# Performance work log

Hardware: AMD Instinct MI355X
Metric: run time of the kernel (lower is better)

## Reference

```python
import jax, jax.numpy as jnp
import numpy as np

H, W, C = 32, 32, 3
KH, KW, KC = 4, 4, 3
SHIFT = (2, 2)
K = 48
M = 200
NH, NW, NC = H // KH, W // KW, C // KC  # 8, 8, 1
NKERNEL = NH * NW * NC                  # 64
NDIM_SUB = KH * KW * KC                 # 48
NDIM = H * W * C                        # 3072
NTR = NKERNEL * K                       # 3072
N = 8192


def setup_inputs() -> dict:
    key = jax.random.key(0)
    ks = jax.random.split(key, 7)
    data = jax.random.normal(ks[0], (N, NDIM), jnp.float32)
    A_raw = jax.random.normal(ks[1], (NKERNEL, NDIM_SUB, K), jnp.float32)
    # RQspline params: knots span roughly [-5, 5]
    x0 = -5.0 + 0.1 * jax.random.normal(ks[2], (NTR, 1), jnp.float32)
    logdx = jnp.log(10.0 / (M - 1)) + 0.1 * jax.random.normal(ks[3], (NTR, M - 1), jnp.float32)
    y0 = -5.0 + 0.1 * jax.random.normal(ks[4], (NTR, 1), jnp.float32)
    logdy = jnp.log(10.0 / (M - 1)) + 0.1 * jax.random.normal(ks[5], (NTR, M - 1), jnp.float32)
    logderiv = 0.1 * jax.random.normal(ks[6], (NTR, M), jnp.float32)
    return {"data": data, "A_raw": A_raw, "x0": x0, "logdx": logdx,
            "y0": y0, "logdy": logdy, "logderiv": logderiv}


def _patch_dims():
    # Shift() is a circular roll of the flat-index image toward the origin
    dim = jnp.arange(NDIM).reshape(H, W, C)
    dim = jnp.roll(dim, shift=(-SHIFT[0], -SHIFT[1]), axis=(0, 1))
    # (NH,KH,NW,KW,C) -> (NH,NW,KH,KW,C) -> (NKERNEL, NDIM_SUB)
    return dim.reshape(NH, KH, NW, KW, C).transpose(0, 2, 1, 3, 4).reshape(NKERNEL, NDIM_SUB)


def orthogonalize(A_raw):
    # per-patch QR with sign fix, as in __init__
    Q, R = jnp.linalg.qr(A_raw)
    sign = jnp.sign(jnp.diagonal(R, axis1=-2, axis2=-1))
    return Q * sign[:, None, :]


def construct_A(A_blocks):
    rows = _patch_dims()                                               # (NKERNEL, NDIM_SUB)
    cols = K * jnp.arange(NKERNEL)[:, None] + jnp.arange(K)[None, :]   # (NKERNEL, K)
    Afull = jnp.zeros((NDIM, NTR), A_blocks.dtype)
    return Afull.at[rows[:, :, None], cols[:, None, :]].set(A_blocks)


def rqspline_forward(x, x0, logdx, y0, logdy, logderiv):
    # monotone rational-quadratic spline (Gregory-Delbourgo), per-dim knots
    xx = jnp.concatenate([x0, x0 + jnp.cumsum(jnp.exp(logdx), axis=1)], axis=1)  # (NTR, M)
    yy = jnp.concatenate([y0, y0 + jnp.cumsum(jnp.exp(logdy), axis=1)], axis=1)
    delta = jnp.exp(logderiv)
    xT = x.T                                              # (NTR, N)
    idx = jax.vmap(jnp.searchsorted)(xx, xT)              # (NTR, N)
    k = jnp.clip(idx - 1, 0, M - 2)
    xK = jnp.take_along_axis(xx, k, axis=1)
    xK1 = jnp.take_along_axis(xx, k + 1, axis=1)
    yK = jnp.take_along_axis(yy, k, axis=1)
    yK1 = jnp.take_along_axis(yy, k + 1, axis=1)
    dK = jnp.take_along_axis(delta, k, axis=1)
    dK1 = jnp.take_along_axis(delta, k + 1, axis=1)
    xi = jnp.clip((xT - xK) / (xK1 - xK), 0.0, 1.0)
    s = (yK1 - yK) / (xK1 - xK)
    xi1 = xi * (1.0 - xi)
    denom = s + (dK1 + dK - 2.0 * s) * xi1
    y_in = yK + (yK1 - yK) * (s * xi * xi + dK * xi1) / denom
    d_in = s * s * (dK1 * xi * xi + 2.0 * s * xi1 + dK * (1.0 - xi) ** 2) / (denom * denom)
    # linear extrapolation with edge derivatives outside the knot range
    below = idx == 0
    above = idx == M
    y_lo = yy[:, :1] + delta[:, :1] * (xT - xx[:, :1])
    y_hi = yy[:, -1:] + delta[:, -1:] * (xT - xx[:, -1:])
    y = jnp.where(below, y_lo, jnp.where(above, y_hi, y_in))
    d = jnp.where(below, delta[:, :1], jnp.where(above, delta[:, -1:], d_in))
    return y.T, jnp.log(d).T                              # (N, NTR) each


def reference(data, A_raw, x0, logdx, y0, logdy, logderiv):
    A = construct_A(orthogonalize(A_raw))                 # (NDIM, NTR) block-structured
    data0 = data @ A                                      # (N, NTR) patch projections
    remaining = data - data0 @ A.T
    y, logd = rqspline_forward(data0, x0, logdx, y0, logdy, logderiv)
    logj = jnp.sum(logd, axis=1)                          # (N,)
    out = remaining + y @ A.T                             # (N, NDIM)
    return out, logj
```

## Files before the change

### kernel.cpp

```cpp
#include <hip/hip_runtime.h>

#define NSMP  8192
#define NDIM  3072
#define NK    64
#define NS    48
#define MK    200
#define GB    256

__device__ __forceinline__ float rcp_fast(float x) { return __builtin_amdgcn_rcpf(x); }
__device__ __forceinline__ int imin(int a, int b) { return a < b ? a : b; }

__global__ __launch_bounds__(64) void qr_kernel(const float* __restrict__ Araw,
                                                float* __restrict__ Qws) {
  const int k = blockIdx.x;
  const int lane = threadIdx.x;
  const float* Ak = Araw + k * NS * NS;
  float col[NS];
#pragma unroll
  for (int r = 0; r < NS; ++r)
    col[r] = (lane < NS) ? Ak[r * NS + lane] : 0.f;

  for (int j = 0; j < NS; ++j) {
    float q[NS];
#pragma unroll
    for (int r = 0; r < NS; ++r)
      q[r] = __int_as_float(__builtin_amdgcn_readlane(__float_as_int(col[r]), j));
    float n0 = 0.f, n1 = 0.f, n2 = 0.f, n3 = 0.f;
#pragma unroll
    for (int r = 0; r < NS; r += 4) {
      n0 = fmaf(q[r+0], q[r+0], n0); n1 = fmaf(q[r+1], q[r+1], n1);
      n2 = fmaf(q[r+2], q[r+2], n2); n3 = fmaf(q[r+3], q[r+3], n3);
    }
    float rinv = 1.0f / sqrtf((n0 + n1) + (n2 + n3));
#pragma unroll
    for (int r = 0; r < NS; ++r) q[r] *= rinv;
    if (lane == j) {
#pragma unroll
      for (int r = 0; r < NS; ++r) col[r] = q[r];
    } else if (lane > j && lane < NS) {
      float d0 = 0.f, d1 = 0.f, d2 = 0.f, d3 = 0.f;
#pragma unroll
      for (int r = 0; r < NS; r += 4) {
        d0 = fmaf(q[r+0], col[r+0], d0); d1 = fmaf(q[r+1], col[r+1], d1);
        d2 = fmaf(q[r+2], col[r+2], d2); d3 = fmaf(q[r+3], col[r+3], d3);
      }
      float dt = (d0 + d1) + (d2 + d3);
#pragma unroll
      for (int r = 0; r < NS; ++r) col[r] = fmaf(-dt, q[r], col[r]);
    }
  }
  if (lane < NS) {
    float* Qk = Qws + k * NS * NS;
#pragma unroll
    for (int r = 0; r < NS; ++r) Qk[r * NS + lane] = col[r];
  }
}

__global__ __launch_bounds__(256) void knots_kernel(
    const float* __restrict__ x0, const float* __restrict__ logdx,
    const float* __restrict__ y0, const float* __restrict__ logdy,
    const float* __restrict__ logderiv,
    float* __restrict__ xxg, float4* __restrict__ ydk8,
    float4* __restrict__ edge, unsigned char* __restrict__ gridb) {
  const int wid = threadIdx.x >> 6, lane = threadIdx.x & 63;
  const int t = blockIdx.x * 4 + wid;
  __shared__ float sxx[4][MK], syy[4][MK], sdel[4][MK];

  {
    const float* row = logdx + t * (MK - 1);
    int i0 = lane * 4;
    float e0 = (i0 + 0 < MK - 1) ? __expf(row[i0 + 0]) : 0.f;
    float e1 = (i0 + 1 < MK - 1) ? __expf(row[i0 + 1]) : 0.f;
    float e2 = (i0 + 2 < MK - 1) ? __expf(row[i0 + 2]) : 0.f;
    float e3 = (i0 + 3 < MK - 1) ? __expf(row[i0 + 3]) : 0.f;
    float p0 = e0, p1 = p0 + e1, p2 = p1 + e2, p3 = p2 + e3;
    float incl = p3;
#pragma unroll
    for (int off = 1; off < 64; off <<= 1) {
      float u = __shfl_up(incl, off, 64);
      if (lane >= off) incl += u;
    }
    float xv = x0[t];
    float base = xv + (incl - p3);
    float* xrow = xxg + t * MK;
    if (lane == 0) { xrow[0] = xv; sxx[wid][0] = xv; }
    if (i0 + 0 < MK - 1) { xrow[1+i0+0] = base + p0; sxx[wid][1+i0+0] = base + p0; }
    if (i0 + 1 < MK - 1) { xrow[1+i0+1] = base + p1; sxx[wid][1+i0+1] = base + p1; }
    if (i0 + 2 < MK - 1) { xrow[1+i0+2] = base + p2; sxx[wid][1+i0+2] = base + p2; }
    if (i0 + 3 < MK - 1) { xrow[1+i0+3] = base + p3; sxx[wid][1+i0+3] = base + p3; }
  }
  {
    const float* row = logdy + t * (MK - 1);
    int i0 = lane * 4;
    float e0 = (i0 + 0 < MK - 1) ? __expf(row[i0 + 0]) : 0.f;
    float e1 = (i0 + 1 < MK - 1) ? __expf(row[i0 + 1]) : 0.f;
    float e2 = (i0 + 2 < MK - 1) ? __expf(row[i0 + 2]) : 0.f;
    float e3 = (i0 + 3 < MK - 1) ? __expf(row[i0 + 3]) : 0.f;
    float p0 = e0, p1 = p0 + e1, p2 = p1 + e2, p3 = p2 + e3;
    float incl = p3;
#pragma unroll
    for (int off = 1; off < 64; off <<= 1) {
      float u = __shfl_up(incl, off, 64);
      if (lane >= off) incl += u;
    }
    float yv = y0[t];
    float base = yv + (incl - p3);
    if (lane == 0) syy[wid][0] = yv;
    if (i0 + 0 < MK - 1) syy[wid][1+i0+0] = base + p0;
    if (i0 + 1 < MK - 1) syy[wid][1+i0+1] = base + p1;
    if (i0 + 2 < MK - 1) syy[wid][1+i0+2] = base + p2;
    if (i0 + 3 < MK - 1) syy[wid][1+i0+3] = base + p3;
  }
  {
    const float* ld = logderiv + t * MK;
#pragma unroll
    for (int rep = 0; rep < 4; ++rep) {
      int m = lane + rep * 64;
      if (m < MK) sdel[wid][m] = __expf(ld[m]);
    }
  }
  __syncthreads();

#pragma unroll
  for (int rep = 0; rep < 4; ++rep) {
    int kk = lane + rep * 64;
    if (kk < MK - 1) {
      float xK = sxx[wid][kk], dx = sxx[wid][kk+1] - xK;
      float yK = syy[wid][kk], dy = syy[wid][kk+1] - yK;
      float rdx = 1.0f / dx;
      float s_ = dy * rdx;
      float dK = sdel[wid][kk], dK1 = sdel[wid][kk+1];
      ydk8[(t * (MK-1) + kk) * 2 + 0] = make_float4(xK, rdx, yK, dy);
      ydk8[(t * (MK-1) + kk) * 2 + 1] = make_float4(s_, dK, dK1, dK + dK1 - 2.f * s_);
    }
  }
  float xx0v = sxx[wid][0], xxMv = sxx[wid][MK-1];
  if (lane == 0) {
    float scale = (float)GB / (xxMv - xx0v);
    edge[t*2+0] = make_float4(xx0v, syy[wid][0],    sdel[wid][0],    scale);
    edge[t*2+1] = make_float4(xxMv, syy[wid][MK-1], sdel[wid][MK-1], 0.f);
  }
  float bw = (xxMv - xx0v) * (1.f / (float)GB);
#pragma unroll
  for (int i = 0; i < 4; ++i) {
    int g = lane * 4 + i;
    float L = xx0v + (float)g * bw;
    int p = 0;
#pragma unroll
    for (int st = 128; st >= 1; st >>= 1) {
      int cand = p + st;
      if (cand < MK && sxx[wid][cand] < L) p = cand;
    }
    gridb[t * GB + g] = (unsigned char)(p > MK-2 ? MK-2 : p);
  }
}

template<int CH>
__global__ __launch_bounds__(256) void gather_kernel(const float* __restrict__ data,
                                                     float* __restrict__ Xg,
                                                     int chunk_base) {
  const int tid = threadIdx.x;
  const int rr = blockIdx.x & 31, tile = blockIdx.x >> 5;
  const int q = (rr + 30) & 31;
  const int nh = q >> 2, kh = q & 3;
  const int n0 = tile * 32;
  __shared__ float sd[32][97];
#pragma unroll
  for (int it = 0; it < 3; ++it) {
    int i = tid + it * 256;
    int s = i / 24, f4 = i % 24;
    float4 v = *(const float4*)(data + (size_t)(chunk_base + n0 + s) * NDIM + rr * 96 + f4 * 4);
    sd[s][f4*4+0] = v.x; sd[s][f4*4+1] = v.y; sd[s][f4*4+2] = v.z; sd[s][f4*4+3] = v.w;
  }
  __syncthreads();
#pragma unroll
  for (int it = 0; it < 3; ++it) {
    int o = tid + it * 256;
    int s4 = o & 7, p = o >> 3;
    int nw = p / 12, dd = p % 12;
    int c = 12 * nw + 6 + dd; c -= (c >= 96) ? 96 : 0;
    int k = nh * 8 + nw, d = kh * 12 + dd;
    float4 v = make_float4(sd[4*s4+0][c], sd[4*s4+1][c], sd[4*s4+2][c], sd[4*s4+3][c]);
    *(float4*)(Xg + ((size_t)(k * NS + d)) * CH + n0 + 4 * s4) = v;
  }
}

template<int CH>
__global__ __launch_bounds__(512, 4) void core_kernel(
    float* __restrict__ Xg, const float* __restrict__ Qws,
    const float* __restrict__ xxg, const unsigned char* __restrict__ gridb,
    const float4* __restrict__ edge, const float4* __restrict__ ydk8,
    float* __restrict__ partial, int chunk_base) {
  const int tid = threadIdx.x;
  const int k = blockIdx.x & 63, tile = blockIdx.x >> 6;
  const int n0 = tile * 128;
  const int lane = tid & 63;
  const int slice = __builtin_amdgcn_readfirstlane(tid >> 7);
  const int shalf = (tid >> 6) & 1;
  const int s = shalf * 64 + lane;

  __shared__ float xs[128][49];
  __shared__ float lp[4][128];

  const float* Qk = Qws + k * NS * NS;

  {
    const int sS = tid & 127, dq = tid >> 7;
    const float* src = Xg + (size_t)k * NS * CH + n0 + sS;
#pragma unroll
    for (int r = 0; r < 12; ++r) {
      int d = dq * 12 + r;
      xs[sS][d] = src[(size_t)d * CH];
    }
  }
  __syncthreads();

  float acc[12];
#pragma unroll
  for (int j = 0; j < 12; ++j) acc[j] = 0.f;
  {
    const float* qbase = Qk + slice * 12;
#pragma unroll 4
    for (int d = 0; d < NS; ++d) {
      float xd = xs[s][d];
      const float* q = qbase + d * NS;
#pragma unroll
      for (int j = 0; j < 12; ++j) acc[j] = fmaf(xd, q[j], acc[j]);
    }
  }

  float logsum = 0.f;
  {
    const unsigned char* gk = gridb + (size_t)k * NS * GB;
    const float4* yk = ydk8 + (size_t)k * NS * (MK - 1) * 2;
    const float4* ek = edge + (size_t)k * NS * 2;
    const float* xk = xxg + (size_t)k * NS * MK;
#pragma unroll
    for (int jj = 0; jj < 12; ++jj) {
      const int jg = slice * 12 + jj;
      float v = acc[jj];
      float4 e0 = ek[2*jg], e1 = ek[2*jg+1];
      int g = (int)((v - e0.x) * e0.w);
      g = g < 0 ? 0 : (g > GB-1 ? GB-1 : g);
      int kk = gk[jg * GB + g];
      const float* xr = xk + jg * MK;
      float xA = xr[imin(kk + 1, MK - 1)];
      float xB = xr[imin(kk + 2, MK - 1)];
      float xC = xr[imin(kk + 3, MK - 1)];
      kk += (int)(kk + 1 <= MK-2 && xA < v) + (int)(kk + 2 <= MK-2 && xB < v)
          + (int)(kk + 3 <= MK-2 && xC < v);
      float4 r0 = yk[(jg * (MK-1) + kk) * 2 + 0];
      float4 r1 = yk[(jg * (MK-1) + kk) * 2 + 1];
      float xi = (v - r0.x) * r0.y;
      xi = fminf(fmaxf(xi, 0.f), 1.f);
      float omxi = 1.f - xi, xi1 = xi * omxi, xi2 = xi * xi;
      float denom = fmaf(r1.w, xi1, r1.x);
      float rden = rcp_fast(denom);
      float y_in = fmaf(r0.w * fmaf(r1.x, xi2, r1.y * xi1), rden, r0.z);
      float d_in = r1.x * r1.x * (r1.z * xi2 + 2.f * r1.x * xi1 + r1.y * omxi * omxi) * (rden * rden);
      bool below = v <= e0.x, above = v > e1.x;
      float yv = below ? fmaf(e0.z, v - e0.x, e0.y)
               : (above ? fmaf(e1.z, v - e1.x, e1.y) : y_in);
      float dd = below ? e0.z : (above ? e1.z : d_in);
      logsum += __logf(dd);
      acc[jj] = yv - v;
    }
  }

  __syncthreads();
#pragma unroll
  for (int jj = 0; jj < 12; ++jj) xs[s][slice * 12 + jj] = acc[jj];
  lp[slice][s] = logsum;
  __syncthreads();

  if (tid < 128) {
    float t = lp[0][tid] + lp[1][tid] + lp[2][tid] + lp[3][tid];
    partial[(size_t)k * NSMP + chunk_base + n0 + tid] = t;
  }

  float r[12];
#pragma unroll
  for (int d = 0; d < 12; ++d) r[d] = 0.f;
  {
    const float* qrow = Qk + (slice * 12) * NS;
#pragma unroll 2
    for (int j = 0; j < NS; ++j) {
      float ej = xs[s][j];
#pragma unroll
      for (int d = 0; d < 12; ++d) r[d] = fmaf(ej, qrow[d * NS + j], r[d]);
    }
  }
  float* dst = Xg + ((size_t)k * NS + slice * 12) * CH + n0 + s;
#pragma unroll
  for (int d = 0; d < 12; ++d) dst[(size_t)d * CH] = r[d];
}

template<int CH>
__global__ __launch_bounds__(256) void scatter_kernel(const float* __restrict__ data,
                                                      const float* __restrict__ R,
                                                      float* __restrict__ out,
                                                      int chunk_base) {
  const int tid = threadIdx.x;
  const int rr = blockIdx.x & 31, tile = blockIdx.x >> 5;
  const int q = (rr + 30) & 31;
  const int nh = q >> 2, kh = q & 3;
  const int n0 = tile * 32;
  __shared__ float sd[32][97];
#pragma unroll
  for (int it = 0; it < 3; ++it) {
    int o = tid + it * 256;
    int s4 = o & 7, p = o >> 3;
    int nw = p / 12, dd = p % 12;
    int c = 12 * nw + 6 + dd; c -= (c >= 96) ? 96 : 0;
    int k = nh * 8 + nw, d = kh * 12 + dd;
    float4 v = *(const float4*)(R + ((size_t)(k * NS + d)) * CH + n0 + 4 * s4);
    sd[4*s4+0][c] = v.x; sd[4*s4+1][c] = v.y; sd[4*s4+2][c] = v.z; sd[4*s4+3][c] = v.w;
  }
  __syncthreads();
#pragma unroll
  for (int it = 0; it < 3; ++it) {
    int i = tid + it * 256;
    int s = i / 24, f4 = i % 24;
    size_t off = (size_t)(chunk_base + n0 + s) * NDIM + rr * 96 + f4 * 4;
    float4 v = *(const float4*)(data + off);
    v.x += sd[s][f4*4+0]; v.y += sd[s][f4*4+1];
    v.z += sd[s][f4*4+2]; v.w += sd[s][f4*4+3];
    *(float4*)(out + off) = v;
  }
}

__global__ __launch_bounds__(256) void reduce_kernel(const float* __restrict__ partial,
                                                     float* __restrict__ logj) {
  int n = blockIdx.x * 256 + threadIdx.x;
  float s = 0.f;
#pragma unroll
  for (int k = 0; k < NK; ++k) s += partial[k * NSMP + n];
  logj[n] = s;
}

template<int CH>
static void run_pipeline(const float* data, const float* Araw, const float* x0,
                         const float* logdx, const float* y0, const float* logdy,
                         const float* logderiv, float* out, float* ws,
                         hipStream_t stream) {
  float*         Qws   = ws;
  float*         xxg   = Qws  + 64 * NS * NS;
  float4*        ydk8  = (float4*)(xxg + 3072 * MK);
  float4*        edge  = ydk8 + 3072 * (MK - 1) * 2;
  unsigned char* gridb = (unsigned char*)(edge + 3072 * 2);
  float*         Xg    = (float*)(gridb + 3072 * GB);
  float*         partial = Xg + (size_t)NK * NS * CH;

  qr_kernel<<<64, 64, 0, stream>>>(Araw, Qws);
  knots_kernel<<<768, 256, 0, stream>>>(x0, logdx, y0, logdy, logderiv,
                                        xxg, ydk8, edge, gridb);
  for (int c = 0; c < NSMP / CH; ++c) {
    const int base = c * CH;
    gather_kernel<CH> <<<CH,          256, 0, stream>>>(data, Xg, base);
    core_kernel<CH>   <<<64*(CH/128), 512, 0, stream>>>(Xg, Qws, xxg, gridb, edge, ydk8,
                                                        partial, base);
    scatter_kernel<CH><<<CH,          256, 0, stream>>>(data, Xg, out, base);
  }
  reduce_kernel<<<32, 256, 0, stream>>>(partial, out + (size_t)NSMP * NDIM);
}

extern "C" void kernel_launch(void* const* d_in, const int* in_sizes, int n_in,
                              void* d_out, int out_size, void* d_ws, size_t ws_size,
                              hipStream_t stream) {
  const float* data     = (const float*)d_in[0];
  const float* Araw     = (const float*)d_in[1];
  const float* x0       = (const float*)d_in[2];
  const float* logdx    = (const float*)d_in[3];
  const float* y0       = (const float*)d_in[4];
  const float* logdy    = (const float*)d_in[5];
  const float* logderiv = (const float*)d_in[6];
  float* out = (float*)d_out;
  float* ws  = (float*)d_ws;

  const size_t fixed = 589824 + 2457600 + 19562496 + 98304 + 786432 + 2097152;
  if (ws_size >= fixed + (size_t)12288 * 8192)
    run_pipeline<8192>(data, Araw, x0, logdx, y0, logdy, logderiv, out, ws, stream);
  else if (ws_size >= fixed + (size_t)12288 * 4096)
    run_pipeline<4096>(data, Araw, x0, logdx, y0, logdy, logderiv, out, ws, stream);
  else
    run_pipeline<2048>(data, Araw, x0, logdx, y0, logdy, logderiv, out, ws, stream);
}
```

Baseline: 533.6 us.

## Fuse gather, core and scatter into one kernel reading data directly

Removes the separate gather and scatter kernels and the intermediate Xg workspace. Each core block now loads its patch pixels straight from the image rows into registers and shared memory, and writes data plus the back-projection straight to the output, with no chunked pipeline. It also adds a repacked copy of Q so the forward projection reads float4 vectors, vectorises the back-projection reads, and remaps block indices to spread work. This cuts global round trips of the intermediate and the extra launches, at the cost of narrow float2 strided accesses to the image.

```diff
diff --git a/kernel.cpp b/kernel.cpp
--- a/kernel.cpp
+++ b/kernel.cpp
@@ -11,7 +11,8 @@
 __device__ __forceinline__ int imin(int a, int b) { return a < b ? a : b; }
 
 __global__ __launch_bounds__(64) void qr_kernel(const float* __restrict__ Araw,
-                                                float* __restrict__ Qws) {
+                                                float* __restrict__ Qws,
+                                                float* __restrict__ Qpack) {
   const int k = blockIdx.x;
   const int lane = threadIdx.x;
   const float* Ak = Araw + k * NS * NS;
@@ -51,8 +52,12 @@
   }
   if (lane < NS) {
     float* Qk = Qws + k * NS * NS;
-#pragma unroll
-    for (int r = 0; r < NS; ++r) Qk[r * NS + lane] = col[r];
+    float* Pk = Qpack + k * NS * NS + (lane / 12) * (NS * 12) + (lane % 12);
+#pragma unroll
+    for (int r = 0; r < NS; ++r) {
+      Qk[r * NS + lane] = col[r];
+      Pk[r * 12] = col[r];
+    }
   }
 }
 
@@ -155,62 +160,37 @@
   }
 }
 
-template<int CH>
-__global__ __launch_bounds__(256) void gather_kernel(const float* __restrict__ data,
-                                                     float* __restrict__ Xg,
-                                                     int chunk_base) {
+__global__ __launch_bounds__(512, 4) void core_fused(
+    const float* __restrict__ data, const float* __restrict__ Qws,
+    const float* __restrict__ Qpack, const float* __restrict__ xxg,
+    const unsigned char* __restrict__ gridb, const float4* __restrict__ edge,
+    const float4* __restrict__ ydk8, float* __restrict__ partial,
+    float* __restrict__ out) {
+  const int w = blockIdx.x;
+  const int b = (w & 7) * ((NSMP / 128) * 64 / 8) + (w >> 3);
+  const int k = b & 63, tile = b >> 6;
+  const int n0 = tile * 128;
   const int tid = threadIdx.x;
-  const int rr = blockIdx.x & 31, tile = blockIdx.x >> 5;
-  const int q = (rr + 30) & 31;
-  const int nh = q >> 2, kh = q & 3;
-  const int n0 = tile * 32;
-  __shared__ float sd[32][97];
-#pragma unroll
-  for (int it = 0; it < 3; ++it) {
-    int i = tid + it * 256;
-    int s = i / 24, f4 = i % 24;
-    float4 v = *(const float4*)(data + (size_t)(chunk_base + n0 + s) * NDIM + rr * 96 + f4 * 4);
-    sd[s][f4*4+0] = v.x; sd[s][f4*4+1] = v.y; sd[s][f4*4+2] = v.z; sd[s][f4*4+3] = v.w;
-  }
-  __syncthreads();
-#pragma unroll
-  for (int it = 0; it < 3; ++it) {
-    int o = tid + it * 256;
-    int s4 = o & 7, p = o >> 3;
-    int nw = p / 12, dd = p % 12;
-    int c = 12 * nw + 6 + dd; c -= (c >= 96) ? 96 : 0;
-    int k = nh * 8 + nw, d = kh * 12 + dd;
-    float4 v = make_float4(sd[4*s4+0][c], sd[4*s4+1][c], sd[4*s4+2][c], sd[4*s4+3][c]);
-    *(float4*)(Xg + ((size_t)(k * NS + d)) * CH + n0 + 4 * s4) = v;
-  }
-}
-
-template<int CH>
-__global__ __launch_bounds__(512, 4) void core_kernel(
-    float* __restrict__ Xg, const float* __restrict__ Qws,
-    const float* __restrict__ xxg, const unsigned char* __restrict__ gridb,
-    const float4* __restrict__ edge, const float4* __restrict__ ydk8,
-    float* __restrict__ partial, int chunk_base) {
-  const int tid = threadIdx.x;
-  const int k = blockIdx.x & 63, tile = blockIdx.x >> 6;
-  const int n0 = tile * 128;
-  const int lane = tid & 63;
+  const int s = tid & 127;
   const int slice = __builtin_amdgcn_readfirstlane(tid >> 7);
-  const int shalf = (tid >> 6) & 1;
-  const int s = shalf * 64 + lane;
 
   __shared__ float xs[128][49];
   __shared__ float lp[4][128];
 
-  const float* Qk = Qws + k * NS * NS;
-
-  {
-    const int sS = tid & 127, dq = tid >> 7;
-    const float* src = Xg + (size_t)k * NS * CH + n0 + sS;
-#pragma unroll
-    for (int r = 0; r < 12; ++r) {
-      int d = dq * 12 + r;
-      xs[sS][d] = src[(size_t)d * CH];
+  const int nh = k >> 3, nw = k & 7;
+  const int r_img = (4 * nh + slice + 2) & 31;
+  const int c0 = 12 * nw + 6;
+
+  float xreg[12];
+  {
+    const float* drow = data + (size_t)(n0 + s) * NDIM + r_img * 96;
+#pragma unroll
+    for (int e = 0; e < 6; ++e) {
+      int col = c0 + 2 * e; col -= (col >= 96) ? 96 : 0;
+      float2 v = *(const float2*)(drow + col);
+      xreg[2*e]   = v.x; xreg[2*e+1] = v.y;
+      xs[s][slice * 12 + 2*e]     = v.x;
+      xs[s][slice * 12 + 2*e + 1] = v.y;
     }
   }
   __syncthreads();
@@ -219,13 +199,17 @@
 #pragma unroll
   for (int j = 0; j < 12; ++j) acc[j] = 0.f;
   {
-    const float* qbase = Qk + slice * 12;
+    const float4* qa = (const float4*)(Qpack + k * NS * NS + slice * (NS * 12));
 #pragma unroll 4
     for (int d = 0; d < NS; ++d) {
       float xd = xs[s][d];
-      const float* q = qbase + d * NS;
-#pragma unroll
-      for (int j = 0; j < 12; ++j) acc[j] = fmaf(xd, q[j], acc[j]);
+      float4 q0 = qa[d*3+0], q1 = qa[d*3+1], q2 = qa[d*3+2];
+      acc[0] = fmaf(xd, q0.x, acc[0]); acc[1] = fmaf(xd, q0.y, acc[1]);
+      acc[2] = fmaf(xd, q0.z, acc[2]); acc[3] = fmaf(xd, q0.w, acc[3]);
+      acc[4] = fmaf(xd, q1.x, acc[4]); acc[5] = fmaf(xd, q1.y, acc[5]);
+      acc[6] = fmaf(xd, q1.z, acc[6]); acc[7] = fmaf(xd, q1.w, acc[7]);
+      acc[8] = fmaf(xd, q2.x, acc[8]); acc[9] = fmaf(xd, q2.y, acc[9]);
+      acc[10]= fmaf(xd, q2.z, acc[10]); acc[11]= fmaf(xd, q2.w, acc[11]);
     }
   }
 
@@ -270,62 +254,40 @@
   __syncthreads();
 #pragma unroll
   for (int jj = 0; jj < 12; ++jj) xs[s][slice * 12 + jj] = acc[jj];
+  __syncthreads();
+
+  float r[12];
+#pragma unroll
+  for (int d = 0; d < 12; ++d) r[d] = 0.f;
+  {
+    const float* qc = Qws + k * NS * NS + (slice * 12) * NS;
+#pragma unroll
+    for (int jc = 0; jc < 12; ++jc) {
+      float ea = xs[s][4*jc+0], eb = xs[s][4*jc+1];
+      float ec = xs[s][4*jc+2], ed = xs[s][4*jc+3];
+#pragma unroll
+      for (int dd = 0; dd < 12; ++dd) {
+        float4 q = *(const float4*)(qc + dd * NS + 4 * jc);
+        r[dd] = fmaf(ed, q.w, fmaf(ec, q.z, fmaf(eb, q.y, fmaf(ea, q.x, r[dd]))));
+      }
+    }
+  }
+
+  {
+    float* orow = out + (size_t)(n0 + s) * NDIM + r_img * 96;
+#pragma unroll
+    for (int e = 0; e < 6; ++e) {
+      int col = c0 + 2 * e; col -= (col >= 96) ? 96 : 0;
+      *(float2*)(orow + col) = make_float2(xreg[2*e] + r[2*e],
+                                           xreg[2*e+1] + r[2*e+1]);
+    }
+  }
+
   lp[slice][s] = logsum;
   __syncthreads();
-
   if (tid < 128) {
     float t = lp[0][tid] + lp[1][tid] + lp[2][tid] + lp[3][tid];
-    partial[(size_t)k * NSMP + chunk_base + n0 + tid] = t;
-  }
-
-  float r[12];
-#pragma unroll
-  for (int d = 0; d < 12; ++d) r[d] = 0.f;
-  {
-    const float* qrow = Qk + (slice * 12) * NS;
-#pragma unroll 2
-    for (int j = 0; j < NS; ++j) {
-      float ej = xs[s][j];
-#pragma unroll
-      for (int d = 0; d < 12; ++d) r[d] = fmaf(ej, qrow[d * NS + j], r[d]);
-    }
-  }
-  float* dst = Xg + ((size_t)k * NS + slice * 12) * CH + n0 + s;
-#pragma unroll
-  for (int d = 0; d < 12; ++d) dst[(size_t)d * CH] = r[d];
-}
-
-template<int CH>
-__global__ __launch_bounds__(256) void scatter_kernel(const float* __restrict__ data,
-                                                      const float* __restrict__ R,
-                                                      float* __restrict__ out,
-                                                      int chunk_base) {
-  const int tid = threadIdx.x;
-  const int rr = blockIdx.x & 31, tile = blockIdx.x >> 5;
-  const int q = (rr + 30) & 31;
-  const int nh = q >> 2, kh = q & 3;
-  const int n0 = tile * 32;
-  __shared__ float sd[32][97];
-#pragma unroll
-  for (int it = 0; it < 3; ++it) {
-    int o = tid + it * 256;
-    int s4 = o & 7, p = o >> 3;
-    int nw = p / 12, dd = p % 12;
-    int c = 12 * nw + 6 + dd; c -= (c >= 96) ? 96 : 0;
-    int k = nh * 8 + nw, d = kh * 12 + dd;
-    float4 v = *(const float4*)(R + ((size_t)(k * NS + d)) * CH + n0 + 4 * s4);
-    sd[4*s4+0][c] = v.x; sd[4*s4+1][c] = v.y; sd[4*s4+2][c] = v.z; sd[4*s4+3][c] = v.w;
-  }
-  __syncthreads();
-#pragma unroll
-  for (int it = 0; it < 3; ++it) {
-    int i = tid + it * 256;
-    int s = i / 24, f4 = i % 24;
-    size_t off = (size_t)(chunk_base + n0 + s) * NDIM + rr * 96 + f4 * 4;
-    float4 v = *(const float4*)(data + off);
-    v.x += sd[s][f4*4+0]; v.y += sd[s][f4*4+1];
-    v.z += sd[s][f4*4+2]; v.w += sd[s][f4*4+3];
-    *(float4*)(out + off) = v;
+    partial[(size_t)k * NSMP + n0 + tid] = t;
   }
 }
 
@@ -336,32 +298,6 @@
 #pragma unroll
   for (int k = 0; k < NK; ++k) s += partial[k * NSMP + n];
   logj[n] = s;
-}
-
-template<int CH>
-static void run_pipeline(const float* data, const float* Araw, const float* x0,
-                         const float* logdx, const float* y0, const float* logdy,
-                         const float* logderiv, float* out, float* ws,
-                         hipStream_t stream) {
-  float*         Qws   = ws;
-  float*         xxg   = Qws  + 64 * NS * NS;
-  float4*        ydk8  = (float4*)(xxg + 3072 * MK);
-  float4*        edge  = ydk8 + 3072 * (MK - 1) * 2;
-  unsigned char* gridb = (unsigned char*)(edge + 3072 * 2);
-  float*         Xg    = (float*)(gridb + 3072 * GB);
-  float*         partial = Xg + (size_t)NK * NS * CH;
-
-  qr_kernel<<<64, 64, 0, stream>>>(Araw, Qws);
-  knots_kernel<<<768, 256, 0, stream>>>(x0, logdx, y0, logdy, logderiv,
-                                        xxg, ydk8, edge, gridb);
-  for (int c = 0; c < NSMP / CH; ++c) {
-    const int base = c * CH;
-    gather_kernel<CH> <<<CH,          256, 0, stream>>>(data, Xg, base);
-    core_kernel<CH>   <<<64*(CH/128), 512, 0, stream>>>(Xg, Qws, xxg, gridb, edge, ydk8,
-                                                        partial, base);
-    scatter_kernel<CH><<<CH,          256, 0, stream>>>(data, Xg, out, base);
-  }
-  reduce_kernel<<<32, 256, 0, stream>>>(partial, out + (size_t)NSMP * NDIM);
 }
 
 extern "C" void kernel_launch(void* const* d_in, const int* in_sizes, int n_in,
@@ -377,11 +313,19 @@
   float* out = (float*)d_out;
   float* ws  = (float*)d_ws;
 
-  const size_t fixed = 589824 + 2457600 + 19562496 + 98304 + 786432 + 2097152;
-  if (ws_size >= fixed + (size_t)12288 * 8192)
-    run_pipeline<8192>(data, Araw, x0, logdx, y0, logdy, logderiv, out, ws, stream);
-  else if (ws_size >= fixed + (size_t)12288 * 4096)
-    run_pipeline<4096>(data, Araw, x0, logdx, y0, logdy, logderiv, out, ws, stream);
-  else
-    run_pipeline<2048>(data, Araw, x0, logdx, y0, logdy, logderiv, out, ws, stream);
-}
+  float*         Qws   = ws;
+  float*         Qpack = Qws + 64 * NS * NS;
+  float*         xxg   = Qpack + 64 * NS * NS;
+  float4*        ydk8  = (float4*)(xxg + 3072 * MK);
+  float4*        edge  = ydk8 + 3072 * (MK - 1) * 2;
+  unsigned char* gridb = (unsigned char*)(edge + 3072 * 2);
+  float*         partial = (float*)(gridb + 3072 * GB);
+
+  qr_kernel<<<64, 64, 0, stream>>>(Araw, Qws, Qpack);
+  knots_kernel<<<768, 256, 0, stream>>>(x0, logdx, y0, logdy, logderiv,
+                                        xxg, ydk8, edge, gridb);
+  core_fused<<<(NSMP / 128) * 64, 512, 0, stream>>>(data, Qws, Qpack, xxg,
+                                                    gridb, edge, ydk8,
+                                                    partial, out);
+  reduce_kernel<<<32, 256, 0, stream>>>(partial, out + (size_t)NSMP * NDIM);
+}
```

Result: slower. 584.7 us (+9.6%).
